# Kernel tuning notes

Hardware: AMD Instinct MI355X
Metric: run time of the kernel (lower is better)

The kernel has to match this reference:

```python
import jax, jax.numpy as jnp
import numpy as np

N, E, IN, H, D = 50000, 800000, 256, 4, 32
ALPHA = 0.2


def setup_inputs() -> dict:
    key = jax.random.key(0)
    ks = jax.random.split(key, 8)
    return {
        "node_feature": jax.random.normal(ks[0], (N, IN), dtype=jnp.float32),
        "edge_feature": jax.random.normal(ks[1], (E, IN), dtype=jnp.float32),
        "src": jax.random.randint(ks[2], (E,), 0, N, dtype=jnp.int32),
        "dst": jax.random.randint(ks[3], (E,), 0, N, dtype=jnp.int32),
        "W": jax.random.normal(ks[4], (IN, H * D), dtype=jnp.float32) * (1.0 / np.sqrt(IN)),
        "attn_l": jax.random.normal(ks[5], (H, D), dtype=jnp.float32),
        "attn_r": jax.random.normal(ks[6], (H, D), dtype=jnp.float32),
        "attn_e": jax.random.normal(ks[7], (H, D), dtype=jnp.float32),
    }


def reference(node_feature, edge_feature, src, dst, W, attn_l, attn_r, attn_e):
    n = node_feature.shape[0]
    h, d = attn_l.shape
    # shared linear projection for node and edge features (feat_drop is identity, p=0)
    ft = (node_feature @ W).reshape(n, h, d)            # [N,H,D]
    e_ft = (edge_feature @ W).reshape(-1, h, d)          # [E,H,D]
    # per-head scalar attention logits
    a1 = jnp.einsum("nhd,hd->nh", ft, attn_l)            # [N,H]
    a2 = jnp.einsum("nhd,hd->nh", ft, attn_r)            # [N,H]
    a3 = jnp.einsum("ehd,hd->eh", e_ft, attn_e)          # [E,H]
    logits = jax.nn.leaky_relu(a1[src] + a3 + a2[dst], negative_slope=ALPHA)  # [E,H]
    # edge softmax grouped by destination node
    m = jax.ops.segment_max(logits, dst, num_segments=n)  # [N,H]
    ex = jnp.exp(logits - m[dst])                        # [E,H]
    s = jax.ops.segment_sum(ex, dst, num_segments=n)     # [N,H]
    a = ex / s[dst]                                       # [E,H] (attn_drop identity)
    # weighted messages: attention-weighted src feats + attention-weighted edge feats
    aw = a[:, :, None]                                    # [E,H,1]
    f_cat = e_ft * aw + ft[src] * aw                      # [E,H,D]
    node_out = jax.ops.segment_sum(f_cat, dst, num_segments=n)  # [N,H,D]
    ret1 = jax.nn.elu(node_out.reshape(n, h * d))
    ret2 = jax.nn.elu(f_cat.reshape(-1, h * d))
    return ret1, ret2
```

## Files before the change

### kernel.cpp

```cpp
#include <hip/hip_runtime.h>
#include <hip/hip_bf16.h>
#include <math.h>

#define NN    50000
#define EE    800000
#define IN_F  256
#define HH    4
#define DD    32
#define OUT_F 128
#define ALPHA 0.2f

typedef float f32x4 __attribute__((ext_vector_type(4)));
typedef short bf16x8 __attribute__((ext_vector_type(8)));

__device__ __forceinline__ float elu_f(float x) { return x > 0.0f ? x : expm1f(x); }

__device__ __forceinline__ unsigned short f2bf(float x) {
    union { float f; unsigned u; } v; v.f = x;
    unsigned r = (v.u + 0x7FFFu + ((v.u >> 16) & 1u)) >> 16;
    return (unsigned short)r;
}
__device__ __forceinline__ float bf2f(unsigned short h) {
    union { unsigned u; float f; } v; v.u = ((unsigned)h) << 16; return v.f;
}

#define PREP_B 128
#define HIST_B 3125
#define SSUM_B 196
#define RET1_B 6250
__global__ __launch_bounds__(256) void k_setup(const float* __restrict__ W,
        unsigned short* __restrict__ Whp, unsigned short* __restrict__ Wlp,
        const int* __restrict__ dst, int* __restrict__ hist,
        float4* __restrict__ ssum4, float4* __restrict__ ret14) {
    const int b = blockIdx.x, tid = threadIdx.x;
    if (b < PREP_B) {
        int i = b * 256 + tid;
        int j = i & 7, lane = (i >> 3) & 63, cf = (i >> 9) & 7, t = i >> 12;
        int krow = 32 * t + 8 * (lane >> 4) + j;
        int col  = 16 * cf + (lane & 15);
        float x = W[krow * OUT_F + col];
        unsigned short h = f2bf(x);
        Whp[i] = h;
        Wlp[i] = f2bf(x - bf2f(h));
    } else if (b < PREP_B + HIST_B) {
        int i = (b - PREP_B) * 256 + tid;
        atomicAdd(&hist[dst[i]], 1);
    } else if (b < PREP_B + HIST_B + SSUM_B) {
        int i = (b - PREP_B - HIST_B) * 256 + tid;
        if (i < NN * HH / 4) ssum4[i] = make_float4(0.f, 0.f, 0.f, 0.f);
    } else {
        int i = (b - PREP_B - HIST_B - SSUM_B) * 256 + tid;
        ret14[i] = make_float4(0.f, 0.f, 0.f, 0.f);
    }
}

template <int MODE>
__global__ __launch_bounds__(256, 4) void k_gemm(const float* __restrict__ X, int M,
        const unsigned short* __restrict__ Whp, const unsigned short* __restrict__ Wlp,
        const float* __restrict__ av0, const float* __restrict__ av1,
        const int* __restrict__ src, const int* __restrict__ dst,
        const float* __restrict__ a1, const float* __restrict__ a2,
        unsigned short* __restrict__ Yh,
        float* __restrict__ o1, float* __restrict__ o2,
        float* __restrict__ ssum) {
    __shared__ unsigned short Asw[2][2][64 * 64];
    __shared__ float p_lds[4][64];
    __shared__ float q_lds[4][64];

    const int tid = threadIdx.x;
    const int w = tid >> 6;
    const int l = tid & 63;
    const int base = blockIdx.x * 64;

    int s_e = 0, t_e = 0;
    if (MODE == 1) { s_e = src[base + l]; t_e = dst[base + l]; }

    const int srow = tid >> 2;
    const int scg  = tid & 3;
    int gr = base + srow; if (gr > M - 1) gr = M - 1;
    const float* xp = X + (size_t)gr * IN_F + scg * 16;

    float4 xs[4];
    #pragma unroll
    for (int q = 0; q < 4; ++q) xs[q] = *(const float4*)(xp + q * 4);

    auto cvtwrite = [&](int buf) {
        unsigned short h[16], lo[16];
        const float* xf = (const float*)xs;
        #pragma unroll
        for (int k = 0; k < 16; ++k) {
            h[k]  = f2bf(xf[k]);
            lo[k] = f2bf(xf[k] - bf2f(h[k]));
        }
        const unsigned sw = (unsigned)((srow & 7) << 4);
        const unsigned b0 = (unsigned)(srow * 128 + scg * 32) ^ sw;
        const unsigned b1 = (unsigned)(srow * 128 + scg * 32 + 16) ^ sw;
        char* ph = (char*)&Asw[buf][0][0];
        char* pl = (char*)&Asw[buf][1][0];
        *(bf16x8*)(ph + b0) = *(const bf16x8*)(h);
        *(bf16x8*)(ph + b1) = *(const bf16x8*)(h + 8);
        *(bf16x8*)(pl + b0) = *(const bf16x8*)(lo);
        *(bf16x8*)(pl + b1) = *(const bf16x8*)(lo + 8);
    };
    cvtwrite(0);

    float a1v = 0.f, a2v = 0.f;
    if (MODE == 1) {
        a1v = a1[(size_t)s_e * HH + w];
        a2v = a2[(size_t)t_e * HH + w];
    }

    f32x4 acc[4][2];
    #pragma unroll
    for (int rf = 0; rf < 4; ++rf)
        #pragma unroll
        for (int cf = 0; cf < 2; ++cf)
            acc[rf][cf] = (f32x4){0.f, 0.f, 0.f, 0.f};

    #pragma unroll
    for (int c = 0; c < 4; ++c) {
        __syncthreads();
        if (c < 3) {
            #pragma unroll
            for (int q = 0; q < 4; ++q)
                xs[q] = *(const float4*)(xp + (c + 1) * 64 + q * 4);
        }
        bf16x8 Bh[2][2], Bl[2][2];
        #pragma unroll
        for (int ks = 0; ks < 2; ++ks)
            #pragma unroll
            for (int cf = 0; cf < 2; ++cf) {
                size_t off = ((size_t)((c * 2 + ks) * 8 + (w * 2 + cf)) * 64 + l) * 8;
                Bh[ks][cf] = *(const bf16x8*)(Whp + off);
                Bl[ks][cf] = *(const bf16x8*)(Wlp + off);
            }
        const char* ph = (const char*)&Asw[c & 1][0][0];
        const char* pl = (const char*)&Asw[c & 1][1][0];
        #pragma unroll
        for (int rf = 0; rf < 4; ++rf) {
            const int row = rf * 16 + (l & 15);
            const unsigned sw = (unsigned)((row & 7) << 4);
            #pragma unroll
            for (int ks = 0; ks < 2; ++ks) {
                const unsigned ba = (unsigned)(row * 128 + ks * 64 + (l >> 4) * 16) ^ sw;
                bf16x8 ah = *(const bf16x8*)(ph + ba);
                bf16x8 al = *(const bf16x8*)(pl + ba);
                #pragma unroll
                for (int cf = 0; cf < 2; ++cf) {
                    acc[rf][cf] = __builtin_amdgcn_mfma_f32_16x16x32_bf16(ah, Bh[ks][cf], acc[rf][cf], 0, 0, 0);
                    acc[rf][cf] = __builtin_amdgcn_mfma_f32_16x16x32_bf16(al, Bh[ks][cf], acc[rf][cf], 0, 0, 0);
                    acc[rf][cf] = __builtin_amdgcn_mfma_f32_16x16x32_bf16(ah, Bl[ks][cf], acc[rf][cf], 0, 0, 0);
                }
            }
        }
        if (c < 3) cvtwrite((c + 1) & 1);
    }

    #pragma unroll
    for (int rf = 0; rf < 4; ++rf)
        #pragma unroll
        for (int cf = 0; cf < 2; ++cf)
            #pragma unroll
            for (int r = 0; r < 4; ++r) {
                int grow = base + rf * 16 + (l >> 4) * 4 + r;
                if (MODE == 1 || grow < M)
                    Yh[(size_t)grow * OUT_F + w * 32 + cf * 16 + (l & 15)] =
                        f2bf(acc[rf][cf][r]);
            }

    const float b0 = av0[w * DD + (l & 15)];
    const float b1 = av0[w * DD + 16 + (l & 15)];
    float c0v = 0.f, c1v = 0.f;
    if (MODE == 0) { c0v = av1[w * DD + (l & 15)]; c1v = av1[w * DD + 16 + (l & 15)]; }

    float pv[4][4], qv[4][4];
    #pragma unroll
    for (int rf = 0; rf < 4; ++rf)
        #pragma unroll
        for (int r = 0; r < 4; ++r) {
            pv[rf][r] = acc[rf][0][r] * b0 + acc[rf][1][r] * b1;
            if (MODE == 0) qv[rf][r] = acc[rf][0][r] * c0v + acc[rf][1][r] * c1v;
        }
    #pragma unroll
    for (int o = 1; o <= 8; o <<= 1)
        #pragma unroll
        for (int rf = 0; rf < 4; ++rf)
            #pragma unroll
            for (int r = 0; r < 4; ++r) {
                pv[rf][r] += __shfl_xor(pv[rf][r], o);
                if (MODE == 0) qv[rf][r] += __shfl_xor(qv[rf][r], o);
            }
    if ((l & 15) == 0) {
        const int hi = l >> 4;
        #pragma unroll
        for (int rf = 0; rf < 4; ++rf)
            #pragma unroll
            for (int r = 0; r < 4; ++r) {
                p_lds[w][rf * 16 + hi * 4 + r] = pv[rf][r];
                if (MODE == 0) q_lds[w][rf * 16 + hi * 4 + r] = qv[rf][r];
            }
    }
    __syncthreads();

    const int grow = base + l;
    if (MODE == 0) {
        if (grow < M) {
            o1[(size_t)grow * HH + w] = p_lds[w][l];
            o2[(size_t)grow * HH + w] = q_lds[w][l];
        }
    } else {
        float lg = p_lds[w][l] + a1v + a2v;
        lg = fmaxf(lg, ALPHA * lg);
        float exv = expf(lg);
        o1[(size_t)grow * HH + w] = exv;
        atomicAdd(&ssum[t_e * HH + w], exv);
    }
}

__global__ __launch_bounds__(1024) void k_scan(const int* __restrict__ hist,
        int* __restrict__ cursor) {
    __shared__ int part[1024];
    const int t = threadIdx.x;
    const int CH = (NN + 1023) / 1024;
    const int b = t * CH;
    int s = 0;
    for (int i = 0; i < CH; ++i) {
        int idx = b + i;
        if (idx < NN) s += hist[idx];
    }
    part[t] = s;
    __syncthreads();
    int total = s;
    for (int o = 1; o < 1024; o <<= 1) {
        int u = (t >= o) ? part[t - o] : 0;
        __syncthreads();
        part[t] += u;
        __syncthreads();
    }
    int run = part[t] - total;
    for (int i = 0; i < CH; ++i) {
        int idx = b + i;
        if (idx < NN) {
            cursor[idx] = run;
            run += hist[idx];
        }
    }
}

__global__ __launch_bounds__(256) void k_scatter(const int* __restrict__ dst,
        int* __restrict__ cursor, int* __restrict__ order) {
    int i = blockIdx.x * 256 + threadIdx.x;
    if (i < EE) {
        int pos = atomicAdd(&cursor[dst[i]], 1);
        order[pos] = i;
    }
}

__global__ __launch_bounds__(256, 8) void k_agg2(const int* __restrict__ order,
        const int* __restrict__ src, const int* __restrict__ dst,
        const unsigned short* __restrict__ ftb, const float* __restrict__ exq,
        const float* __restrict__ ssum, const unsigned short* __restrict__ eftb,
        float* __restrict__ ret2, float* __restrict__ node_out) {
    __shared__ int eL[64], sL[64], dL[64];
    __shared__ int sent[2];
    const int tid = threadIdx.x;
    const int base = blockIdx.x * 64;
    if (tid < 64) {
        int e = order[base + tid];
        eL[tid] = e;
        sL[tid] = src[e];
        dL[tid] = dst[e];
    } else if (tid == 64) {
        sent[0] = (blockIdx.x > 0) ? dst[order[base - 1]] : -1;
    } else if (tid == 65) {
        sent[1] = (base + 64 < EE) ? dst[order[base + 64]] : -1;
    }
    __syncthreads();

    const int w = tid >> 6, l = tid & 63;
    const int W0 = w * 16, W1 = W0 + 15;
    const int c0 = l * 2, h = l >> 4;

    const int dprev  = (W0 == 0)  ? sent[0] : dL[W0 - 1];
    const int dafter = (W1 == 63) ? sent[1] : dL[W1 + 1];

    float acc0 = 0.f, acc1 = 0.f;
    int dcur = dL[W0];
    bool touch_start = true;

    #pragma unroll 4
    for (int r = W0; r <= W1; ++r) {
        const int e = eL[r], s = sL[r], d = dL[r];
        if (d != dcur) {
            const size_t o = (size_t)dcur * OUT_F + c0;
            if (touch_start && dcur == dprev) {
                atomicAdd(&node_out[o], acc0);
                atomicAdd(&node_out[o + 1], acc1);
            } else {
                *(float2*)(node_out + o) = make_float2(acc0, acc1);
            }
            acc0 = acc1 = 0.f; dcur = d; touch_start = false;
        }
        const float a = exq[(size_t)e * HH + h] * __frcp_rn(ssum[d * HH + h]);
        ushort2 ev = *(const ushort2*)(eftb + (size_t)e * OUT_F + c0);
        ushort2 fv = *(const ushort2*)(ftb + (size_t)s * OUT_F + c0);
        float f0 = (bf2f(ev.x) + bf2f(fv.x)) * a;
        float f1 = (bf2f(ev.y) + bf2f(fv.y)) * a;
        acc0 += f0; acc1 += f1;
        *(float2*)(ret2 + (size_t)e * OUT_F + c0) = make_float2(elu_f(f0), elu_f(f1));
    }
    {
        const size_t o = (size_t)dcur * OUT_F + c0;
        const bool at = (touch_start && dcur == dprev) || (dcur == dafter);
        if (at) {
            atomicAdd(&node_out[o], acc0);
            atomicAdd(&node_out[o + 1], acc1);
        } else {
            *(float2*)(node_out + o) = make_float2(acc0, acc1);
        }
    }
}

__global__ __launch_bounds__(256) void k_elu1(const float4* __restrict__ node_out,
        float4* __restrict__ ret1) {
    const int i = blockIdx.x * blockDim.x + threadIdx.x;
    if (i < NN * OUT_F / 4) {
        float4 v = node_out[i];
        ret1[i] = make_float4(elu_f(v.x), elu_f(v.y), elu_f(v.z), elu_f(v.w));
    }
}

extern "C" void kernel_launch(void* const* d_in, const int* in_sizes, int n_in,
                              void* d_out, int out_size, void* d_ws, size_t ws_size,
                              hipStream_t stream) {
    const float* nf     = (const float*)d_in[0];
    const float* ef     = (const float*)d_in[1];
    const int*   src    = (const int*)d_in[2];
    const int*   dst    = (const int*)d_in[3];
    const float* W      = (const float*)d_in[4];
    const float* attn_l = (const float*)d_in[5];
    const float* attn_r = (const float*)d_in[6];
    const float* attn_e = (const float*)d_in[7];

    float* ret1 = (float*)d_out;
    float* ret2 = ret1 + (size_t)NN * OUT_F;

    char* wsp = (char*)d_ws;
    auto take = [&](size_t bytes) { char* p = wsp; wsp += (bytes + 511) & ~size_t(511); return p; };
    unsigned short* ftb = (unsigned short*)take((size_t)NN * OUT_F * 2);
    float* a1buf  = (float*)take((size_t)NN * HH * 4);
    float* a2buf  = (float*)take((size_t)NN * HH * 4);
    float* exq    = (float*)take((size_t)EE * HH * 4);
    float* ssum   = (float*)take((size_t)NN * HH * 4);
    unsigned short* Whp = (unsigned short*)take(32768 * 2);
    unsigned short* Wlp = (unsigned short*)take(32768 * 2);
    int* hist   = (int*)take((size_t)NN * 4);
    int* cursor = (int*)take((size_t)NN * 4);
    int* order  = (int*)take((size_t)EE * 4);
    unsigned short* eftb = (unsigned short*)take((size_t)EE * OUT_F * 2);

    hipMemsetAsync(hist, 0, (size_t)NN * 4, stream);
    k_setup<<<PREP_B + HIST_B + SSUM_B + RET1_B, 256, 0, stream>>>(
            W, Whp, Wlp, dst, hist, (float4*)ssum, (float4*)ret1);
    k_scan<<<1, 1024, 0, stream>>>(hist, cursor);
    k_scatter<<<(EE + 255) / 256, 256, 0, stream>>>(dst, cursor, order);

    k_gemm<0><<<(NN + 63) / 64, 256, 0, stream>>>(nf, NN, Whp, Wlp,
            attn_l, attn_r, nullptr, nullptr, nullptr, nullptr,
            ftb, a1buf, a2buf, nullptr);
    k_gemm<1><<<EE / 64, 256, 0, stream>>>(ef, EE, Whp, Wlp,
            attn_e, nullptr, src, dst, a1buf, a2buf,
            eftb, exq, nullptr, ssum);

    k_agg2<<<EE / 64, 256, 0, stream>>>(order, src, dst, ftb, exq, ssum,
                                        eftb, ret2, ret1);
    k_elu1<<<(NN * OUT_F / 4 + 255) / 256, 256, 0, stream>>>(
            (const float4*)ret1, (float4*)ret1);
}
```

Baseline: 756.0 us.

## Fuse histogram into node GEMM and scatter into edge GEMM launches

Histogram building now runs as extra blocks inside the node-projection GEMM launch, and the counting-sort scatter runs as extra blocks inside the edge GEMM launch. The hipMemsetAsync is replaced by zeroing hist in the setup kernel. Shared memory is merged into one 32KB buffer reused for the reduction scratch, with the edge kernel's launch bounds raised to 5 blocks per CU. This removes launches and lets the atomic-heavy index work overlap with the matrix work, at the cost of more register and LDS pressure and of mixing different workloads within a single grid.

Measured after the change: 778.1 us. 1.03x slower.

```diff
diff --git a/kernel.cpp b/kernel.cpp
--- a/kernel.cpp
+++ b/kernel.cpp
@@ -10,6 +10,11 @@
 #define OUT_F 128
 #define ALPHA 0.2f
 
+#define NODE_GB 782
+#define EDGE_GB 12500
+#define HIST_GB 3125
+#define SCAT_GB 3125
+
 typedef float f32x4 __attribute__((ext_vector_type(4)));
 typedef short bf16x8 __attribute__((ext_vector_type(8)));
 
@@ -25,13 +30,13 @@
 }
 
 #define PREP_B 128
-#define HIST_B 3125
-#define SSUM_B 196
-#define RET1_B 6250
-__global__ __launch_bounds__(256) void k_setup(const float* __restrict__ W,
+#define ZH_B   49
+#define ZS_B   196
+#define ZR_B   6250
+__global__ __launch_bounds__(256) void k_setup0(const float* __restrict__ W,
         unsigned short* __restrict__ Whp, unsigned short* __restrict__ Wlp,
-        const int* __restrict__ dst, int* __restrict__ hist,
-        float4* __restrict__ ssum4, float4* __restrict__ ret14) {
+        int4* __restrict__ hist4, float4* __restrict__ ssum4,
+        float4* __restrict__ ret14) {
     const int b = blockIdx.x, tid = threadIdx.x;
     if (b < PREP_B) {
         int i = b * 256 + tid;
@@ -42,20 +47,21 @@
         unsigned short h = f2bf(x);
         Whp[i] = h;
         Wlp[i] = f2bf(x - bf2f(h));
-    } else if (b < PREP_B + HIST_B) {
+    } else if (b < PREP_B + ZH_B) {
         int i = (b - PREP_B) * 256 + tid;
-        atomicAdd(&hist[dst[i]], 1);
-    } else if (b < PREP_B + HIST_B + SSUM_B) {
-        int i = (b - PREP_B - HIST_B) * 256 + tid;
-        if (i < NN * HH / 4) ssum4[i] = make_float4(0.f, 0.f, 0.f, 0.f);
+        if (i < 12500) hist4[i] = make_int4(0, 0, 0, 0);
+    } else if (b < PREP_B + ZH_B + ZS_B) {
+        int i = (b - PREP_B - ZH_B) * 256 + tid;
+        if (i < 50000) ssum4[i] = make_float4(0.f, 0.f, 0.f, 0.f);
     } else {
-        int i = (b - PREP_B - HIST_B - SSUM_B) * 256 + tid;
+        int i = (b - PREP_B - ZH_B - ZS_B) * 256 + tid;
         ret14[i] = make_float4(0.f, 0.f, 0.f, 0.f);
     }
 }
 
 template <int MODE>
-__global__ __launch_bounds__(256, 4) void k_gemm(const float* __restrict__ X, int M,
+__device__ __forceinline__ void gemm_body(int bid, const float* __restrict__ X,
+        int M,
         const unsigned short* __restrict__ Whp, const unsigned short* __restrict__ Wlp,
         const float* __restrict__ av0, const float* __restrict__ av1,
         const int* __restrict__ src, const int* __restrict__ dst,
@@ -63,14 +69,12 @@
         unsigned short* __restrict__ Yh,
         float* __restrict__ o1, float* __restrict__ o2,
         float* __restrict__ ssum) {
-    __shared__ unsigned short Asw[2][2][64 * 64];
-    __shared__ float p_lds[4][64];
-    __shared__ float q_lds[4][64];
+    __shared__ char smem[32768];
 
     const int tid = threadIdx.x;
     const int w = tid >> 6;
     const int l = tid & 63;
-    const int base = blockIdx.x * 64;
+    const int base = bid * 64;
 
     int s_e = 0, t_e = 0;
     if (MODE == 1) { s_e = src[base + l]; t_e = dst[base + l]; }
@@ -95,8 +99,8 @@
         const unsigned sw = (unsigned)((srow & 7) << 4);
         const unsigned b0 = (unsigned)(srow * 128 + scg * 32) ^ sw;
         const unsigned b1 = (unsigned)(srow * 128 + scg * 32 + 16) ^ sw;
-        char* ph = (char*)&Asw[buf][0][0];
-        char* pl = (char*)&Asw[buf][1][0];
+        char* ph = smem + (buf * 2 + 0) * 8192;
+        char* pl = smem + (buf * 2 + 1) * 8192;
         *(bf16x8*)(ph + b0) = *(const bf16x8*)(h);
         *(bf16x8*)(ph + b1) = *(const bf16x8*)(h + 8);
         *(bf16x8*)(pl + b0) = *(const bf16x8*)(lo);
@@ -134,8 +138,8 @@
                 Bh[ks][cf] = *(const bf16x8*)(Whp + off);
                 Bl[ks][cf] = *(const bf16x8*)(Wlp + off);
             }
-        const char* ph = (const char*)&Asw[c & 1][0][0];
-        const char* pl = (const char*)&Asw[c & 1][1][0];
+        const char* ph = smem + ((c & 1) * 2 + 0) * 8192;
+        const char* pl = smem + ((c & 1) * 2 + 1) * 8192;
         #pragma unroll
         for (int rf = 0; rf < 4; ++rf) {
             const int row = rf * 16 + (l & 15);
@@ -190,14 +194,18 @@
                 pv[rf][r] += __shfl_xor(pv[rf][r], o);
                 if (MODE == 0) qv[rf][r] += __shfl_xor(qv[rf][r], o);
             }
+
+    float* p_lds = (float*)smem;
+    float* q_lds = (float*)(smem + 1024);
+    __syncthreads();
     if ((l & 15) == 0) {
         const int hi = l >> 4;
         #pragma unroll
         for (int rf = 0; rf < 4; ++rf)
             #pragma unroll
             for (int r = 0; r < 4; ++r) {
-                p_lds[w][rf * 16 + hi * 4 + r] = pv[rf][r];
-                if (MODE == 0) q_lds[w][rf * 16 + hi * 4 + r] = qv[rf][r];
+                p_lds[w * 64 + rf * 16 + hi * 4 + r] = pv[rf][r];
+                if (MODE == 0) q_lds[w * 64 + rf * 16 + hi * 4 + r] = qv[rf][r];
             }
     }
     __syncthreads();
@@ -205,15 +213,49 @@
     const int grow = base + l;
     if (MODE == 0) {
         if (grow < M) {
-            o1[(size_t)grow * HH + w] = p_lds[w][l];
-            o2[(size_t)grow * HH + w] = q_lds[w][l];
+            o1[(size_t)grow * HH + w] = p_lds[w * 64 + l];
+            o2[(size_t)grow * HH + w] = q_lds[w * 64 + l];
         }
     } else {
-        float lg = p_lds[w][l] + a1v + a2v;
+        float lg = p_lds[w * 64 + l] + a1v + a2v;
         lg = fmaxf(lg, ALPHA * lg);
         float exv = expf(lg);
         o1[(size_t)grow * HH + w] = exv;
         atomicAdd(&ssum[t_e * HH + w], exv);
+    }
+}
+
+__global__ __launch_bounds__(256, 4) void k_ng(const float* __restrict__ nf,
+        const unsigned short* __restrict__ Whp, const unsigned short* __restrict__ Wlp,
+        const float* __restrict__ attn_l, const float* __restrict__ attn_r,
+        unsigned short* __restrict__ ftb,
+        float* __restrict__ a1buf, float* __restrict__ a2buf,
+        const int* __restrict__ dst, int* __restrict__ hist) {
+    if (blockIdx.x < NODE_GB) {
+        gemm_body<0>(blockIdx.x, nf, NN, Whp, Wlp, attn_l, attn_r,
+                     nullptr, nullptr, nullptr, nullptr,
+                     ftb, a1buf, a2buf, nullptr);
+    } else {
+        int i = (blockIdx.x - NODE_GB) * 256 + threadIdx.x;
+        atomicAdd(&hist[dst[i]], 1);
+    }
+}
+
+__global__ __launch_bounds__(256, 5) void k_eg(const float* __restrict__ ef,
+        const unsigned short* __restrict__ Whp, const unsigned short* __restrict__ Wlp,
+        const float* __restrict__ attn_e,
+        const int* __restrict__ src, const int* __restrict__ dst,
+        const float* __restrict__ a1buf, const float* __restrict__ a2buf,
+        unsigned short* __restrict__ eftb, float* __restrict__ exq,
+        float* __restrict__ ssum,
+        int* __restrict__ cursor, int* __restrict__ order) {
+    if (blockIdx.x < EDGE_GB) {
+        gemm_body<1>(blockIdx.x, ef, EE, Whp, Wlp, attn_e, nullptr,
+                     src, dst, a1buf, a2buf, eftb, exq, nullptr, ssum);
+    } else {
+        int i = (blockIdx.x - EDGE_GB) * 256 + threadIdx.x;
+        int pos = atomicAdd(&cursor[dst[i]], 1);
+        order[pos] = i;
     }
 }
 
@@ -244,15 +286,6 @@
             cursor[idx] = run;
             run += hist[idx];
         }
-    }
-}
-
-__global__ __launch_bounds__(256) void k_scatter(const int* __restrict__ dst,
-        int* __restrict__ cursor, int* __restrict__ order) {
-    int i = blockIdx.x * 256 + threadIdx.x;
-    if (i < EE) {
-        int pos = atomicAdd(&cursor[dst[i]], 1);
-        order[pos] = i;
     }
 }
 
@@ -354,24 +387,18 @@
     float* ssum   = (float*)take((size_t)NN * HH * 4);
     unsigned short* Whp = (unsigned short*)take(32768 * 2);
     unsigned short* Wlp = (unsigned short*)take(32768 * 2);
-    int* hist   = (int*)take((size_t)NN * 4);
+    int* hist   = (int*)take((size_t)(NN + 16) * 4);
     int* cursor = (int*)take((size_t)NN * 4);
     int* order  = (int*)take((size_t)EE * 4);
     unsigned short* eftb = (unsigned short*)take((size_t)EE * OUT_F * 2);
 
-    hipMemsetAsync(hist, 0, (size_t)NN * 4, stream);
-    k_setup<<<PREP_B + HIST_B + SSUM_B + RET1_B, 256, 0, stream>>>(
-            W, Whp, Wlp, dst, hist, (float4*)ssum, (float4*)ret1);
+    k_setup0<<<PREP_B + ZH_B + ZS_B + ZR_B, 256, 0, stream>>>(
+            W, Whp, Wlp, (int4*)hist, (float4*)ssum, (float4*)ret1);
+    k_ng<<<NODE_GB + HIST_GB, 256, 0, stream>>>(nf, Whp, Wlp, attn_l, attn_r,
+            ftb, a1buf, a2buf, dst, hist);
     k_scan<<<1, 1024, 0, stream>>>(hist, cursor);
-    k_scatter<<<(EE + 255) / 256, 256, 0, stream>>>(dst, cursor, order);
-
-    k_gemm<0><<<(NN + 63) / 64, 256, 0, stream>>>(nf, NN, Whp, Wlp,
-            attn_l, attn_r, nullptr, nullptr, nullptr, nullptr,
-            ftb, a1buf, a2buf, nullptr);
-    k_gemm<1><<<EE / 64, 256, 0, stream>>>(ef, EE, Whp, Wlp,
-            attn_e, nullptr, src, dst, a1buf, a2buf,
-            eftb, exq, nullptr, ssum);
-
+    k_eg<<<EDGE_GB + SCAT_GB, 256, 0, stream>>>(ef, Whp, Wlp, attn_e,
+            src, dst, a1buf, a2buf, eftb, exq, ssum, cursor, order);
     k_agg2<<<EE / 64, 256, 0, stream>>>(order, src, dst, ftb, exq, ssum,
                                         eftb, ret2, ret1);
     k_elu1<<<(NN * OUT_F / 4 + 255) / 256, 256, 0, stream>>>(
```
